# Optimization experiments

Measured on AMD Instinct MI355X. Metric: run time of the kernel, lower is better.

## Reference

```python
import jax, jax.numpy as jnp
import numpy as np

GRAVITY = 9.81007  # pypose default, gravity vector [0,0,g]

# Quaternions are xyzw (pypose SO3 convention). q1*q2 composes rotations R1@R2.

def qmul(q1, q2):
    v1, w1 = q1[..., :3], q1[..., 3:]
    v2, w2 = q2[..., :3], q2[..., 3:]
    w = w1 * w2 - jnp.sum(v1 * v2, axis=-1, keepdims=True)
    v = w1 * v2 + w2 * v1 + jnp.cross(v1, v2)
    return jnp.concatenate([v, w], axis=-1)

def qinv(q):
    return jnp.concatenate([-q[..., :3], q[..., 3:]], axis=-1)

def qrot(q, v):
    # rotate vector v by unit quaternion q: v + 2*cross(qv, cross(qv,v) + qw*v)
    qv, qw = q[..., :3], q[..., 3:]
    t = jnp.cross(qv, v) + qw * v
    return v + 2.0 * jnp.cross(qv, t)

def so3_exp(phi):
    # so3 -> SO3 quaternion: q = [phi*sin(|phi|/2)/|phi|, cos(|phi|/2)]
    theta = jnp.linalg.norm(phi, axis=-1, keepdims=True)
    small = theta < 1e-6
    safe = jnp.where(small, 1.0, theta)
    k = jnp.where(small, 0.5 - theta * theta / 48.0, jnp.sin(0.5 * theta) / safe)
    return jnp.concatenate([phi * k, jnp.cos(0.5 * theta)], axis=-1)


def setup_inputs() -> dict:
    key = jax.random.key(0)
    ks = jax.random.split(key, 7)
    B, F = 64, 32768
    dt = jax.random.uniform(ks[0], (B, F, 1), jnp.float32) * 0.01 + 0.004
    gyro = jax.random.normal(ks[1], (B, F, 3), jnp.float32) * 0.1
    acc = jax.random.normal(ks[2], (B, F, 3), jnp.float32)

    def rand_quat(k, shape):
        q = jax.random.normal(k, shape + (4,), jnp.float32)
        return q / jnp.linalg.norm(q, axis=-1, keepdims=True)

    gt_rot = rand_quat(ks[3], (B, F))      # ground-truth orientations (xyzw)
    init_rot = rand_quat(ks[4], (B, 1))
    init_vel = jax.random.normal(ks[5], (B, 1, 3), jnp.float32)
    init_pos = jax.random.normal(ks[6], (B, 1, 3), jnp.float32)
    return dict(dt=dt, gyro=gyro, acc=acc, gt_rot=gt_rot,
                init_rot=init_rot, init_vel=init_vel, init_pos=init_pos)


def reference(dt, gyro, acc, gt_rot, init_rot, init_vel, init_pos):
    # IMU preintegration (pypose IMUPreintegrator, reset=True, prop_cov=False,
    # training branch: gravity removed in body frame via ground-truth rot).
    g = jnp.array([0.0, 0.0, GRAVITY], dtype=dt.dtype)
    dr = so3_exp(gyro * dt)                                   # (B,F,4) per-step rotation
    # cumulative rotation increment: incre_r[i] = dr_0 * dr_1 * ... * dr_i
    incre_r = jax.lax.associative_scan(qmul, dr, axis=1)      # (B,F,4)
    # gravity-compensated body-frame acceleration
    a = acc - qrot(qinv(gt_rot), g)                           # (B,F,3)
    ra = qrot(incre_r, a)                                     # rotated into init frame
    incre_v = jnp.cumsum(ra * dt, axis=1)                     # (B,F,3)
    v_prev = jnp.concatenate([jnp.zeros_like(incre_v[:, :1]), incre_v[:, :-1]], axis=1)
    incre_p = jnp.cumsum(v_prev * dt + 0.5 * ra * dt * dt, axis=1)
    incre_t = jnp.cumsum(dt, axis=1)                          # (B,F,1)
    # compose with initial state
    rot = qmul(init_rot, incre_r)                             # (B,F,4)
    vel = init_vel + qrot(init_rot, incre_v)                  # (B,F,3)
    pos = init_pos + init_vel * incre_t + qrot(init_rot, incre_p)  # (B,F,3)
    return rot, vel, pos
```

## Files before the change

kernel.cpp:

```cpp
#include <hip/hip_runtime.h>
#include <math.h>

namespace {

constexpr int SEQ    = 4;
constexpr int WCHUNK = 64 * SEQ;
constexpr int BELEMS = 1024;

constexpr int GY_F  = 0;
constexpr int AC_F  = 3072;
constexpr int GT_F  = 6144;
constexpr int LDS_F = 10240;

struct V3 { float x, y, z; };
struct Q4 { float x, y, z, w; };
struct St { Q4 q; V3 s; V3 p; float T; float pad; };

__device__ __forceinline__ Q4 qmul(const Q4 a, const Q4 b) {
  Q4 r;
  r.x = a.w*b.x + b.w*a.x + a.y*b.z - a.z*b.y;
  r.y = a.w*b.y + b.w*a.y + a.z*b.x - a.x*b.z;
  r.z = a.w*b.z + b.w*a.z + a.x*b.y - a.y*b.x;
  r.w = a.w*b.w - a.x*b.x - a.y*b.y - a.z*b.z;
  return r;
}

__device__ __forceinline__ V3 qrot(const Q4 q, const V3 v) {
  float tx = q.y*v.z - q.z*v.y + q.w*v.x;
  float ty = q.z*v.x - q.x*v.z + q.w*v.y;
  float tz = q.x*v.y - q.y*v.x + q.w*v.z;
  V3 r;
  r.x = v.x + 2.0f*(q.y*tz - q.z*ty);
  r.y = v.y + 2.0f*(q.z*tx - q.x*tz);
  r.z = v.z + 2.0f*(q.x*ty - q.y*tx);
  return r;
}

__device__ __forceinline__ St combine(const St a, const St b) {
  St r;
  r.q = qmul(a.q, b.q);
  V3 rs = qrot(a.q, b.s);
  r.s.x = a.s.x + rs.x;
  r.s.y = a.s.y + rs.y;
  r.s.z = a.s.z + rs.z;
  V3 rp = qrot(a.q, b.p);
  r.p.x = a.p.x + a.s.x*b.T + rp.x;
  r.p.y = a.p.y + a.s.y*b.T + rp.y;
  r.p.z = a.p.z + a.s.z*b.T + rp.z;
  r.T = a.T + b.T;
  r.pad = 0.0f;
  return r;
}

__device__ __forceinline__ St identity_st() {
  St r;
  r.q = {0.0f, 0.0f, 0.0f, 1.0f};
  r.s = {0.0f, 0.0f, 0.0f};
  r.p = {0.0f, 0.0f, 0.0f};
  r.T = 0.0f; r.pad = 0.0f;
  return r;
}

__device__ __forceinline__ St elem_state(float dt, V3 w, V3 ac, Q4 gt) {
  float px = w.x*dt, py = w.y*dt, pz = w.z*dt;
  float t2 = px*px + py*py + pz*pz;
  float k  = 0.5f + t2*(-1.0f/48.0f  + t2*(1.0f/3840.0f));
  float cw = 1.0f + t2*(-0.125f      + t2*(1.0f/384.0f));
  Q4 dr = { px*k, py*k, pz*k, cw };
  Q4 gi = { -gt.x, -gt.y, -gt.z, gt.w };
  V3 g  = { 0.0f, 0.0f, 9.81007f };
  V3 gr = qrot(gi, g);
  V3 a  = { ac.x - gr.x, ac.y - gr.y, ac.z - gr.z };
  V3 ra = qrot(dr, a);
  St e;
  e.q = dr;
  e.s.x = ra.x*dt; e.s.y = ra.y*dt; e.s.z = ra.z*dt;
  float h = 0.5f*dt;
  e.p.x = e.s.x*h; e.p.y = e.s.y*h; e.p.z = e.s.z*h;
  e.T = dt; e.pad = 0.0f;
  return e;
}

__device__ __forceinline__ St recon(float qx, float qy, float qz,
                                    float sx, float sy, float sz, float dt) {
  St e;
  e.q = { qx, qy, qz, sqrtf(fmaxf(1.0f - qx*qx - qy*qy - qz*qz, 0.0f)) };
  e.s = { sx, sy, sz };
  float h = 0.5f*dt;
  e.p = { sx*h, sy*h, sz*h };
  e.T = dt; e.pad = 0.0f;
  return e;
}

__device__ __forceinline__ St shfl_up_st(const St& v, int d) {
  St r;
  r.q.x = __shfl_up(v.q.x, d); r.q.y = __shfl_up(v.q.y, d);
  r.q.z = __shfl_up(v.q.z, d); r.q.w = __shfl_up(v.q.w, d);
  r.s.x = __shfl_up(v.s.x, d); r.s.y = __shfl_up(v.s.y, d);
  r.s.z = __shfl_up(v.s.z, d);
  r.p.x = __shfl_up(v.p.x, d); r.p.y = __shfl_up(v.p.y, d);
  r.p.z = __shfl_up(v.p.z, d);
  r.T   = __shfl_up(v.T, d);   r.pad = 0.0f;
  return r;
}

__device__ __forceinline__ St shfl_down_st(const St& v, int d) {
  St r;
  r.q.x = __shfl_down(v.q.x, d); r.q.y = __shfl_down(v.q.y, d);
  r.q.z = __shfl_down(v.q.z, d); r.q.w = __shfl_down(v.q.w, d);
  r.s.x = __shfl_down(v.s.x, d); r.s.y = __shfl_down(v.s.y, d);
  r.s.z = __shfl_down(v.s.z, d);
  r.p.x = __shfl_down(v.p.x, d); r.p.y = __shfl_down(v.p.y, d);
  r.p.z = __shfl_down(v.p.z, d);
  r.T   = __shfl_down(v.T, d);   r.pad = 0.0f;
  return r;
}

__device__ __forceinline__ St bcast_st(const St& v, int src) {
  St r;
  r.q.x = __shfl(v.q.x, src); r.q.y = __shfl(v.q.y, src);
  r.q.z = __shfl(v.q.z, src); r.q.w = __shfl(v.q.w, src);
  r.s.x = __shfl(v.s.x, src); r.s.y = __shfl(v.s.y, src);
  r.s.z = __shfl(v.s.z, src);
  r.p.x = __shfl(v.p.x, src); r.p.y = __shfl(v.p.y, src);
  r.p.z = __shfl(v.p.z, src);
  r.T   = __shfl(v.T, src);   r.pad = 0.0f;
  return r;
}

__device__ __forceinline__ float4& L4(float* lds, int fidx) {
  int a = fidx << 2;
  a ^= ((a >> 8) & 3) << 4;
  return *reinterpret_cast<float4*>(reinterpret_cast<char*>(lds) + a);
}

__global__ __launch_bounds__(256) void k_agg(
    const float* __restrict__ dtp, const float* __restrict__ gyp,
    const float* __restrict__ acp, const float* __restrict__ gtp,
    St* __restrict__ aggs)
{
  __shared__ __align__(16) float lds[LDS_F];
  const int t = threadIdx.x;
  const int lane = t & 63;
  const size_t base = (size_t)blockIdx.x * BELEMS;

  const float4* ggy = (const float4*)(gyp + base*3);
  const float4* gac = (const float4*)(acp + base*3);
  const float4* ggt = (const float4*)(gtp + base*4);
  #pragma unroll
  for (int k = 0; k < 3; ++k) L4(lds, GY_F + 4*(t + 256*k)) = ggy[t + 256*k];
  #pragma unroll
  for (int k = 0; k < 3; ++k) L4(lds, AC_F + 4*(t + 256*k)) = gac[t + 256*k];
  #pragma unroll
  for (int k = 0; k < 4; ++k) L4(lds, GT_F + 4*(t + 256*k)) = ggt[t + 256*k];
  float4 dt4 = ((const float4*)(dtp + base))[t];
  __syncthreads();

  float gy[12], ac[12], gq[16];
  #pragma unroll
  for (int j = 0; j < 3; ++j) ((float4*)gy)[j] = L4(lds, GY_F + 12*t + 4*j);
  #pragma unroll
  for (int j = 0; j < 3; ++j) ((float4*)ac)[j] = L4(lds, AC_F + 12*t + 4*j);
  #pragma unroll
  for (int j = 0; j < 4; ++j) ((float4*)gq)[j] = L4(lds, GT_F + 16*t + 4*j);
  const float dtv[4] = {dt4.x, dt4.y, dt4.z, dt4.w};

  St run;
  #pragma unroll
  for (int i = 0; i < SEQ; ++i) {
    St e = elem_state(dtv[i],
               {gy[3*i], gy[3*i+1], gy[3*i+2]},
               {ac[3*i], ac[3*i+1], ac[3*i+2]},
               {gq[4*i], gq[4*i+1], gq[4*i+2], gq[4*i+3]});
    if (i == 0) run = e; else run = combine(run, e);
  }
  #pragma unroll
  for (int d = 1; d < 64; d <<= 1) run = combine(run, shfl_down_st(run, d));
  if (lane == 0) aggs[blockIdx.x*4 + (t >> 6)] = run;
}

__global__ __launch_bounds__(64) void k_pref(
    const St* __restrict__ aggs, const float* __restrict__ irp,
    float* __restrict__ prefb, int cpb)
{
  const int b = blockIdx.x;
  const int lane = threadIdx.x & 63;

  St carry = identity_st();
  carry.q = { irp[b*4+0], irp[b*4+1], irp[b*4+2], irp[b*4+3] };

  const int nw = (cpb + 63) >> 6;
  for (int w = 0; w < nw; ++w) {
    const int idx = (w << 6) + lane;
    St A = identity_st();
    if (idx < cpb) A = aggs[(size_t)b*cpb + idx];
    #pragma unroll
    for (int d = 1; d < 64; d <<= 1) {
      St o = shfl_up_st(A, d);
      if (lane >= d) A = combine(o, A);
    }
    St ex = shfl_up_st(A, 1);
    St P = (lane == 0) ? carry : combine(carry, ex);
    if (idx < cpb) {
      float4* pp = (float4*)(prefb + ((size_t)b*cpb + idx)*12);
      pp[0] = make_float4(P.q.x, P.q.y, P.q.z, P.q.w);
      pp[1] = make_float4(P.s.x, P.s.y, P.s.z, P.p.x);
      pp[2] = make_float4(P.p.y, P.p.z, P.T, 0.0f);
    }
    carry = combine(carry, bcast_st(A, 63));
  }
}

__global__ __launch_bounds__(256) void k_emit(
    const float* __restrict__ dtp, const float* __restrict__ gyp,
    const float* __restrict__ acp, const float* __restrict__ gtp,
    const float* __restrict__ prefb,
    const float* __restrict__ ivp, const float* __restrict__ ipp,
    float* __restrict__ out, int F, int cpb, int B)
{
  __shared__ __align__(16) float lds[LDS_F];
  const int t = threadIdx.x;
  const int lane = t & 63;
  const int cid  = blockIdx.x*4 + (t >> 6);
  const int b = cid / cpb;
  const size_t base = (size_t)blockIdx.x * BELEMS;

  St P;
  {
    const float4* pp = (const float4*)(prefb + (size_t)cid*12);
    float4 a = pp[0], bb = pp[1], cc = pp[2];
    P.q = {a.x, a.y, a.z, a.w};
    P.s = {bb.x, bb.y, bb.z};
    P.p = {bb.w, cc.x, cc.y};
    P.T = cc.z; P.pad = 0.0f;
  }

  const float4* ggy = (const float4*)(gyp + base*3);
  const float4* gac = (const float4*)(acp + base*3);
  const float4* ggt = (const float4*)(gtp + base*4);
  #pragma unroll
  for (int k = 0; k < 3; ++k) L4(lds, GY_F + 4*(t + 256*k)) = ggy[t + 256*k];
  #pragma unroll
  for (int k = 0; k < 3; ++k) L4(lds, AC_F + 4*(t + 256*k)) = gac[t + 256*k];
  #pragma unroll
  for (int k = 0; k < 4; ++k) L4(lds, GT_F + 4*(t + 256*k)) = ggt[t + 256*k];
  float4 dt4 = ((const float4*)(dtp + base))[t];
  __syncthreads();

  float cq[SEQ*3], cs[SEQ*3], cdt[SEQ];
  St run;
  {
    float gy[12], ac[12], gq[16];
    #pragma unroll
    for (int j = 0; j < 3; ++j) ((float4*)gy)[j] = L4(lds, GY_F + 12*t + 4*j);
    #pragma unroll
    for (int j = 0; j < 3; ++j) ((float4*)ac)[j] = L4(lds, AC_F + 12*t + 4*j);
    #pragma unroll
    for (int j = 0; j < 4; ++j) ((float4*)gq)[j] = L4(lds, GT_F + 16*t + 4*j);
    const float dtv[4] = {dt4.x, dt4.y, dt4.z, dt4.w};
    #pragma unroll
    for (int i = 0; i < SEQ; ++i) {
      St e = elem_state(dtv[i],
                 {gy[3*i], gy[3*i+1], gy[3*i+2]},
                 {ac[3*i], ac[3*i+1], ac[3*i+2]},
                 {gq[4*i], gq[4*i+1], gq[4*i+2], gq[4*i+3]});
      cq[3*i] = e.q.x; cq[3*i+1] = e.q.y; cq[3*i+2] = e.q.z;
      cs[3*i] = e.s.x; cs[3*i+1] = e.s.y; cs[3*i+2] = e.s.z;
      cdt[i]  = e.T;
      if (i == 0) run = e; else run = combine(run, e);
    }
  }

  St incl = run;
  #pragma unroll
  for (int d = 1; d < 64; d <<= 1) {
    St o = shfl_up_st(incl, d);
    if (lane >= d) incl = combine(o, incl);
  }
  {
    St ex = shfl_up_st(incl, 1);
    if (lane > 0) P = combine(P, ex);
  }

  V3 iv = { ivp[b*3+0], ivp[b*3+1], ivp[b*3+2] };
  V3 ip = { ipp[b*3+0], ipp[b*3+1], ipp[b*3+2] };

  __syncthreads();

  {
    St acc = P;
    float velb[SEQ*3], posb[SEQ*3];
    #pragma unroll
    for (int i = 0; i < SEQ; ++i) {
      St e = recon(cq[3*i], cq[3*i+1], cq[3*i+2],
                   cs[3*i], cs[3*i+1], cs[3*i+2], cdt[i]);
      acc = combine(acc, e);
      L4(lds, GT_F + 4*(4*t + i)) =
          make_float4(acc.q.x, acc.q.y, acc.q.z, acc.q.w);
      velb[3*i+0] = iv.x + acc.s.x;
      velb[3*i+1] = iv.y + acc.s.y;
      velb[3*i+2] = iv.z + acc.s.z;
      posb[3*i+0] = ip.x + iv.x*acc.T + acc.p.x;
      posb[3*i+1] = ip.y + iv.y*acc.T + acc.p.y;
      posb[3*i+2] = ip.z + iv.z*acc.T + acc.p.z;
    }
    #pragma unroll
    for (int j = 0; j < 3; ++j) L4(lds, GY_F + 12*t + 4*j) = ((float4*)velb)[j];
    #pragma unroll
    for (int j = 0; j < 3; ++j) L4(lds, AC_F + 12*t + 4*j) = ((float4*)posb)[j];
  }
  __syncthreads();

  const size_t BF = (size_t)B * (size_t)F;
  float4* grot = (float4*)out + base;
  float4* gvel = (float4*)(out + BF*4 + base*3);
  float4* gpos = (float4*)(out + BF*7 + base*3);
  #pragma unroll
  for (int k = 0; k < 4; ++k) grot[t + 256*k] = L4(lds, GT_F + 4*(t + 256*k));
  #pragma unroll
  for (int k = 0; k < 3; ++k) gvel[t + 256*k] = L4(lds, GY_F + 4*(t + 256*k));
  #pragma unroll
  for (int k = 0; k < 3; ++k) gpos[t + 256*k] = L4(lds, AC_F + 4*(t + 256*k));
}

}

extern "C" void kernel_launch(void* const* d_in, const int* in_sizes, int n_in,
                              void* d_out, int out_size, void* d_ws, size_t ws_size,
                              hipStream_t stream)
{
  (void)n_in; (void)out_size; (void)ws_size;

  const float* dtp = (const float*)d_in[0];
  const float* gyp = (const float*)d_in[1];
  const float* acp = (const float*)d_in[2];
  const float* gtp = (const float*)d_in[3];
  const float* irp = (const float*)d_in[4];
  const float* ivp = (const float*)d_in[5];
  const float* ipp = (const float*)d_in[6];
  float* out = (float*)d_out;

  const int B   = in_sizes[4] / 4;
  const int F   = in_sizes[0] / B;
  const int cpb = F / WCHUNK;
  const int nchunk = B * cpb;

  St*    aggs  = (St*)d_ws;
  float* prefb = (float*)((char*)d_ws + (size_t)nchunk * sizeof(St));

  k_agg <<<nchunk/4, 256, 0, stream>>>(dtp, gyp, acp, gtp, aggs);
  k_pref<<<B,         64, 0, stream>>>(aggs, irp, prefb, cpb);
  k_emit<<<nchunk/4, 256, 0, stream>>>(dtp, gyp, acp, gtp, prefb, ivp, ipp,
                                       out, F, cpb, B);
}
```

Measured before the change: 66.44 us.

## Stage inputs via direct global-to-LDS loads and tree-combine per-thread elements

```diff
diff --git a/kernel.cpp b/kernel.cpp
--- a/kernel.cpp
+++ b/kernel.cpp
@@ -128,11 +128,29 @@
   return r;
 }
 
+__device__ __forceinline__ int swz(int byteoff) {
+  return byteoff ^ (((byteoff >> 8) & 3) << 4);
+}
 __device__ __forceinline__ float4& L4(float* lds, int fidx) {
-  int a = fidx << 2;
-  a ^= ((a >> 8) & 3) << 4;
-  return *reinterpret_cast<float4*>(reinterpret_cast<char*>(lds) + a);
-}
+  return *reinterpret_cast<float4*>(reinterpret_cast<char*>(lds) + swz(fidx << 2));
+}
+
+__device__ __forceinline__ void stage16(const void* gsrc, void* ldst) {
+  __builtin_amdgcn_global_load_lds(
+      (const __attribute__((address_space(1))) void*)gsrc,
+      (__attribute__((address_space(3))) void*)ldst, 16, 0, 0);
+}
+
+#define STAGE_REGION(gbase, regionByte, nK)                                    \
+  {                                                                            \
+    _Pragma("unroll")                                                          \
+    for (int k = 0; k < (nK); ++k) {                                           \
+      int db = (t + 256*k) * 16;                                               \
+      const char* src = (const char*)(gbase) + swz(db);                        \
+      char* ldst = (char*)lds + (regionByte) + (t >> 6)*1024 + k*4096;         \
+      stage16(src, ldst);                                                      \
+    }                                                                          \
+  }
 
 __global__ __launch_bounds__(256) void k_agg(
     const float* __restrict__ dtp, const float* __restrict__ gyp,
@@ -144,15 +162,9 @@
   const int lane = t & 63;
   const size_t base = (size_t)blockIdx.x * BELEMS;
 
-  const float4* ggy = (const float4*)(gyp + base*3);
-  const float4* gac = (const float4*)(acp + base*3);
-  const float4* ggt = (const float4*)(gtp + base*4);
-  #pragma unroll
-  for (int k = 0; k < 3; ++k) L4(lds, GY_F + 4*(t + 256*k)) = ggy[t + 256*k];
-  #pragma unroll
-  for (int k = 0; k < 3; ++k) L4(lds, AC_F + 4*(t + 256*k)) = gac[t + 256*k];
-  #pragma unroll
-  for (int k = 0; k < 4; ++k) L4(lds, GT_F + 4*(t + 256*k)) = ggt[t + 256*k];
+  STAGE_REGION(gyp + base*3, 0,     3);
+  STAGE_REGION(acp + base*3, 12288, 3);
+  STAGE_REGION(gtp + base*4, 24576, 4);
   float4 dt4 = ((const float4*)(dtp + base))[t];
   __syncthreads();
 
@@ -165,15 +177,15 @@
   for (int j = 0; j < 4; ++j) ((float4*)gq)[j] = L4(lds, GT_F + 16*t + 4*j);
   const float dtv[4] = {dt4.x, dt4.y, dt4.z, dt4.w};
 
-  St run;
-  #pragma unroll
-  for (int i = 0; i < SEQ; ++i) {
-    St e = elem_state(dtv[i],
+  St e[SEQ];
+  #pragma unroll
+  for (int i = 0; i < SEQ; ++i)
+    e[i] = elem_state(dtv[i],
                {gy[3*i], gy[3*i+1], gy[3*i+2]},
                {ac[3*i], ac[3*i+1], ac[3*i+2]},
                {gq[4*i], gq[4*i+1], gq[4*i+2], gq[4*i+3]});
-    if (i == 0) run = e; else run = combine(run, e);
-  }
+  St run = combine(combine(e[0], e[1]), combine(e[2], e[3]));
+
   #pragma unroll
   for (int d = 1; d < 64; d <<= 1) run = combine(run, shfl_down_st(run, d));
   if (lane == 0) aggs[blockIdx.x*4 + (t >> 6)] = run;
@@ -234,16 +246,12 @@
     P.p = {bb.w, cc.x, cc.y};
     P.T = cc.z; P.pad = 0.0f;
   }
-
-  const float4* ggy = (const float4*)(gyp + base*3);
-  const float4* gac = (const float4*)(acp + base*3);
-  const float4* ggt = (const float4*)(gtp + base*4);
-  #pragma unroll
-  for (int k = 0; k < 3; ++k) L4(lds, GY_F + 4*(t + 256*k)) = ggy[t + 256*k];
-  #pragma unroll
-  for (int k = 0; k < 3; ++k) L4(lds, AC_F + 4*(t + 256*k)) = gac[t + 256*k];
-  #pragma unroll
-  for (int k = 0; k < 4; ++k) L4(lds, GT_F + 4*(t + 256*k)) = ggt[t + 256*k];
+  V3 iv = { ivp[b*3+0], ivp[b*3+1], ivp[b*3+2] };
+  V3 ip = { ipp[b*3+0], ipp[b*3+1], ipp[b*3+2] };
+
+  STAGE_REGION(gyp + base*3, 0,     3);
+  STAGE_REGION(acp + base*3, 12288, 3);
+  STAGE_REGION(gtp + base*4, 24576, 4);
   float4 dt4 = ((const float4*)(dtp + base))[t];
   __syncthreads();
 
@@ -258,17 +266,18 @@
     #pragma unroll
     for (int j = 0; j < 4; ++j) ((float4*)gq)[j] = L4(lds, GT_F + 16*t + 4*j);
     const float dtv[4] = {dt4.x, dt4.y, dt4.z, dt4.w};
+    St e[SEQ];
     #pragma unroll
     for (int i = 0; i < SEQ; ++i) {
-      St e = elem_state(dtv[i],
+      e[i] = elem_state(dtv[i],
                  {gy[3*i], gy[3*i+1], gy[3*i+2]},
                  {ac[3*i], ac[3*i+1], ac[3*i+2]},
                  {gq[4*i], gq[4*i+1], gq[4*i+2], gq[4*i+3]});
-      cq[3*i] = e.q.x; cq[3*i+1] = e.q.y; cq[3*i+2] = e.q.z;
-      cs[3*i] = e.s.x; cs[3*i+1] = e.s.y; cs[3*i+2] = e.s.z;
-      cdt[i]  = e.T;
-      if (i == 0) run = e; else run = combine(run, e);
+      cq[3*i] = e[i].q.x; cq[3*i+1] = e[i].q.y; cq[3*i+2] = e[i].q.z;
+      cs[3*i] = e[i].s.x; cs[3*i+1] = e[i].s.y; cs[3*i+2] = e[i].s.z;
+      cdt[i]  = e[i].T;
     }
+    run = combine(combine(e[0], e[1]), combine(e[2], e[3]));
   }
 
   St incl = run;
@@ -281,9 +290,6 @@
     St ex = shfl_up_st(incl, 1);
     if (lane > 0) P = combine(P, ex);
   }
-
-  V3 iv = { ivp[b*3+0], ivp[b*3+1], ivp[b*3+2] };
-  V3 ip = { ipp[b*3+0], ipp[b*3+1], ipp[b*3+2] };
 
   __syncthreads();
 
```

Result: slower. 67.91 us (+2.2%).
